# Performance work log

Hardware: AMD Instinct MI355X
Metric: run time of the kernel (lower is better)

## Reference

```python
import jax, jax.numpy as jnp
import numpy as np

B = 512
T = 64
D_MODEL = 1024
N_HEADS = 16
DH = D_MODEL // N_HEADS
GRID_H, GRID_W = 8, 8
DX_MAX, DY_MAX = GRID_W - 1, GRID_H - 1
NUM_REL = (2 * DX_MAX + 1) * (2 * DY_MAX + 1)  # 225


def _build_rel_index():
    # Exactly mirrors RelSelfAttention2DShaw._build_rel_index for an 8x8 board.
    yy, xx = np.meshgrid(np.arange(GRID_H), np.arange(GRID_W), indexing='ij')
    coords = np.stack([xx.reshape(-1), yy.reshape(-1)], axis=-1)  # [T, 2] (x, y)
    disp = coords[None, :, :] - coords[:, None, :]                # [T, T, 2]
    dx = np.clip(disp[..., 0], -DX_MAX, DX_MAX) + DX_MAX
    dy = np.clip(disp[..., 1], -DY_MAX, DY_MAX) + DY_MAX
    return (dx + (2 * DX_MAX + 1) * dy).astype(np.int32)          # [T, T]


def setup_inputs() -> dict:
    key = jax.random.key(0)
    ks = jax.random.split(key, 12)
    w_std = 0.02
    inp = {
        'x':    jax.random.normal(ks[0], (B, T, D_MODEL), dtype=jnp.float32),
        'Wq_w': jax.random.normal(ks[1], (D_MODEL, D_MODEL), dtype=jnp.float32) * w_std,
        'Wq_b': jax.random.normal(ks[2], (D_MODEL,), dtype=jnp.float32) * w_std,
        'Wk_w': jax.random.normal(ks[3], (D_MODEL, D_MODEL), dtype=jnp.float32) * w_std,
        'Wk_b': jax.random.normal(ks[4], (D_MODEL,), dtype=jnp.float32) * w_std,
        'Wv_w': jax.random.normal(ks[5], (D_MODEL, D_MODEL), dtype=jnp.float32) * w_std,
        'Wv_b': jax.random.normal(ks[6], (D_MODEL,), dtype=jnp.float32) * w_std,
        'Wo_w': jax.random.normal(ks[7], (D_MODEL, D_MODEL), dtype=jnp.float32) * w_std,
        'Wo_b': jax.random.normal(ks[8], (D_MODEL,), dtype=jnp.float32) * w_std,
        'rel_q': jax.random.normal(ks[9],  (N_HEADS, NUM_REL, DH), dtype=jnp.float32) * w_std,
        'rel_k': jax.random.normal(ks[10], (N_HEADS, NUM_REL, DH), dtype=jnp.float32) * w_std,
        'rel_v': jax.random.normal(ks[11], (N_HEADS, NUM_REL, DH), dtype=jnp.float32) * w_std,
        'rel_index': jnp.asarray(_build_rel_index()),
    }
    return inp


def reference(x, Wq_w, Wq_b, Wk_w, Wk_b, Wv_w, Wv_b, Wo_w, Wo_b,
              rel_q, rel_k, rel_v, rel_index):
    Bc, Tc, D = x.shape
    H, dh = N_HEADS, DH
    scale = 1.0 / jnp.sqrt(jnp.asarray(dh, dtype=x.dtype))

    # Projections (nn.Linear uses y = x @ W.T + b), split into heads: [B, H, T, dh]
    q = (x @ Wq_w.T + Wq_b).reshape(Bc, Tc, H, dh).transpose(0, 2, 1, 3)
    k = (x @ Wk_w.T + Wk_b).reshape(Bc, Tc, H, dh).transpose(0, 2, 1, 3)
    v = (x @ Wv_w.T + Wv_b).reshape(Bc, Tc, H, dh).transpose(0, 2, 1, 3)

    # Gather per-displacement relative embeddings: [H, T, T, dh]
    rq = rel_q[:, rel_index]
    rk = rel_k[:, rel_index]
    rv = rel_v[:, rel_index]

    # e_ij = (q_i + aQ_ij) . (k_j + aK_ij) / sqrt(dh), expanded into 4 terms
    qk = jnp.einsum('bhtd,bhsd->bhts', q, k)
    q_relk = jnp.einsum('bhtd,htsd->bhts', q, rk)
    relq_k = jnp.einsum('htsd,bhsd->bhts', rq, k)
    relq_relk = jnp.einsum('htsd,htsd->hts', rq, rk)
    logits = (qk + q_relk + relq_k + relq_relk[None]) * scale

    attn = jax.nn.softmax(logits, axis=-1)  # [B, H, T, T]

    # z_i = sum_j attn_ij * (v_j + aV_ij)
    out_v = jnp.einsum('bhts,bhsd->bhtd', attn, v)
    out_relv = jnp.einsum('bhts,htsd->bhtd', attn, rv)
    out = (out_v + out_relv).transpose(0, 2, 1, 3).reshape(Bc, Tc, D)
    return out @ Wo_w.T + Wo_b


if __name__ == '__main__':
    y = reference(**setup_inputs())
    print(y.shape, y.dtype)
```

## Files before the change

kernel.cpp:

```cpp
#include <hip/hip_runtime.h>
#include <cstdint>


typedef unsigned short u16;
typedef unsigned int u32;
typedef __bf16 bf16x8 __attribute__((ext_vector_type(8)));
typedef float f32x4 __attribute__((ext_vector_type(4)));

#define MFMA16(a, b, c) __builtin_amdgcn_mfma_f32_16x16x32_bf16(a, b, c, 0, 0, 0)

__device__ __forceinline__ u16 f2bf(float f) {
  u32 u = __builtin_bit_cast(u32, f);
  u = (u + 0x7FFFu + ((u >> 16) & 1u)) >> 16;
  return (u16)u;
}
__device__ __forceinline__ float bf2f(u16 h) {
  return __builtin_bit_cast(float, ((u32)h) << 16);
}

__device__ __forceinline__ void g2l16(const void* g, void* lds_wave_base) {
#if __has_builtin(__builtin_amdgcn_global_load_lds)
  __builtin_amdgcn_global_load_lds(
      (const __attribute__((address_space(1))) u32*)(uintptr_t)g,
      (__attribute__((address_space(3))) u32*)(uintptr_t)lds_wave_base, 16, 0, 0);
#else
  uint4 v = *(const uint4*)g;
  *(uint4*)((char*)lds_wave_base + (threadIdx.x & 63) * 16) = v;
#endif
}

__global__ __launch_bounds__(256) void k_cvt(const float* __restrict__ src,
                                             u16* __restrict__ dst, int nq) {
  int i = blockIdx.x * 256 + threadIdx.x;
  if (i >= nq) return;
  float4 v = ((const float4*)src)[i];
  ushort4 o;
  o.x = f2bf(v.x); o.y = f2bf(v.y); o.z = f2bf(v.z); o.w = f2bf(v.w);
  ((ushort4*)dst)[i] = o;
}


__device__ __forceinline__ void stageA(const u16* __restrict__ A, int row0,
                                       int kb, char* lds, int buf, int half,
                                       int tid) {
#pragma unroll
  for (int g = 0; g < 2; g++) {
    int ch = g * 512 + tid;
    int sub = ch >> 3, sl = ch & 7;
    int R = (sub & 63) | (half << 6) | ((sub & 64) << 1);
    int kg = sl ^ (sub & 7);
    g2l16(A + (size_t)(row0 + R) * 1024 + kb + kg * 8,
          lds + (buf * 2 + half) * 16384 + g * 8192 + (tid >> 6) * 1024);
  }
}
__device__ __forceinline__ void stageB(const u16* __restrict__ Bm, int col0,
                                       int kb, char* lds, int buf, int half,
                                       int tid) {
#pragma unroll
  for (int g = 0; g < 2; g++) {
    int ch = g * 512 + tid;
    int sub = ch >> 3, sl = ch & 7;
    int C = (sub & 31) | (half << 5) | ((sub & 0x60) << 1);
    int kg = sl ^ (sub & 7);
    g2l16(Bm + (size_t)(col0 + C) * 1024 + kb + kg * 8,
          lds + 65536 + (buf * 2 + half) * 16384 + g * 8192 + (tid >> 6) * 1024);
  }
}

template <int CBUF, int MH, int NH, int RA, int RB, int USEA, int SMAT,
          int SHALF, int SBUF, int KADD, int VMn>
__device__ __forceinline__ void phz(const u16* __restrict__ A,
                                    const u16* __restrict__ Bm, int row0,
                                    int col0, int k0, char* lds,
                                    f32x4 (&acc)[8][4], bf16x8 (&afA)[4][2],
                                    bf16x8 (&afC)[4][2], bf16x8 (&bfB)[2][2],
                                    const int* abase, const int* bbase,
                                    int tid, bool st) {
  if (RA) {
#pragma unroll
    for (int m = 0; m < 4; m++)
#pragma unroll
      for (int kk = 0; kk < 2; kk++) {
        bf16x8 v = *(const bf16x8*)(lds + abase[kk] +
                                    ((CBUF * 2 + MH) * 16384 + m * 2048));
        if (RA == 1) afA[m][kk] = v; else afC[m][kk] = v;
      }
  }
  if (RB) {
#pragma unroll
    for (int n = 0; n < 2; n++)
#pragma unroll
      for (int kk = 0; kk < 2; kk++)
        bfB[n][kk] = *(const bf16x8*)(lds + bbase[kk] +
                                      ((CBUF * 2 + NH) * 16384 + n * 2048));
  }
  if (st) {
    if (SMAT == 0)
      stageA(A, row0, k0 + KADD * 64, lds, SBUF, SHALF, tid);
    else
      stageB(Bm, col0, k0 + KADD * 64, lds, SBUF, SHALF, tid);
  }
  __builtin_amdgcn_s_barrier();
  asm volatile("s_waitcnt lgkmcnt(0)" ::: "memory");
  __builtin_amdgcn_sched_barrier(0);
  __builtin_amdgcn_s_setprio(1);
#pragma unroll
  for (int m = 0; m < 4; m++)
#pragma unroll
    for (int n = 0; n < 2; n++)
#pragma unroll
      for (int kk = 0; kk < 2; kk++)
        acc[MH * 4 + m][NH * 2 + n] = MFMA16(USEA ? afC[m][kk] : afA[m][kk],
                                             bfB[n][kk],
                                             acc[MH * 4 + m][NH * 2 + n]);
  __builtin_amdgcn_s_setprio(0);
  if constexpr (VMn == 8) asm volatile("s_waitcnt vmcnt(8)" ::: "memory");
  else if constexpr (VMn == 6) asm volatile("s_waitcnt vmcnt(6)" ::: "memory");
  else if constexpr (VMn == 4) asm volatile("s_waitcnt vmcnt(4)" ::: "memory");
  else if constexpr (VMn == 2) asm volatile("s_waitcnt vmcnt(2)" ::: "memory");
  else if constexpr (VMn == 0) asm volatile("s_waitcnt vmcnt(0)" ::: "memory");
  __builtin_amdgcn_s_barrier();
}

__device__ __forceinline__ void gemm256_core(const u16* __restrict__ A,
                                             const u16* __restrict__ Bm,
                                             int row0, int col0, char* lds,
                                             f32x4 (&acc)[8][4], int tid) {
  const int lane = tid & 63, w = tid >> 6;
  const int wr = w >> 2, wc = w & 3;
  const int l15 = lane & 15, l4 = lane >> 4;
  const int l7 = l15 & 7;
  int abase[2], bbase[2];
#pragma unroll
  for (int kk = 0; kk < 2; kk++) {
    int swz = ((kk * 4 + l4) ^ l7) << 4;
    abase[kk] = wr * 8192 + l15 * 128 + swz;
    bbase[kk] = 65536 + wc * 4096 + l15 * 128 + swz;
  }
  bf16x8 afA[4][2], afC[4][2], bfB[2][2];
  stageA(A, row0, 0, lds, 0, 0, tid);
  stageB(Bm, col0, 0, lds, 0, 0, tid);
  stageA(A, row0, 0, lds, 0, 1, tid);
  stageB(Bm, col0, 0, lds, 0, 1, tid);
  stageB(Bm, col0, 64, lds, 1, 0, tid);
  stageA(A, row0, 64, lds, 1, 1, tid);
  asm volatile("s_waitcnt vmcnt(4)" ::: "memory");
  __builtin_amdgcn_s_barrier();
  for (int u = 0; u < 7; ++u) {
    int k0 = u * 128;
    phz<0,0,0,1,1,0, 0,0,1,1,-1>(A,Bm,row0,col0,k0,lds,acc,afA,afC,bfB,abase,bbase,tid,true);
    phz<0,1,0,2,0,1, 1,1,1,1, 8>(A,Bm,row0,col0,k0,lds,acc,afA,afC,bfB,abase,bbase,tid,true);
    phz<0,1,1,0,1,1, 1,0,0,2,-1>(A,Bm,row0,col0,k0,lds,acc,afA,afC,bfB,abase,bbase,tid,true);
    phz<0,0,1,0,0,0, 0,1,0,2, 6>(A,Bm,row0,col0,k0,lds,acc,afA,afC,bfB,abase,bbase,tid,true);
    phz<1,0,0,1,1,0, 0,0,0,2,-1>(A,Bm,row0,col0,k0,lds,acc,afA,afC,bfB,abase,bbase,tid,true);
    phz<1,1,0,2,0,1, 1,1,0,2, 8>(A,Bm,row0,col0,k0,lds,acc,afA,afC,bfB,abase,bbase,tid,true);
    phz<1,1,1,0,1,1, 1,0,1,3,-1>(A,Bm,row0,col0,k0,lds,acc,afA,afC,bfB,abase,bbase,tid,true);
    phz<1,0,1,0,0,0, 0,1,1,3, 6>(A,Bm,row0,col0,k0,lds,acc,afA,afC,bfB,abase,bbase,tid,true);
  }
  {
    const int k0 = 896;
    phz<0,0,0,1,1,0, 0,0,1,1,-1>(A,Bm,row0,col0,k0,lds,acc,afA,afC,bfB,abase,bbase,tid,true);
    phz<0,1,0,2,0,1, 1,1,1,1, 8>(A,Bm,row0,col0,k0,lds,acc,afA,afC,bfB,abase,bbase,tid,true);
    phz<0,1,1,0,1,1, 0,0,0,0,-1>(A,Bm,row0,col0,k0,lds,acc,afA,afC,bfB,abase,bbase,tid,false);
    phz<0,0,1,0,0,0, 0,0,0,0, 2>(A,Bm,row0,col0,k0,lds,acc,afA,afC,bfB,abase,bbase,tid,false);
    phz<1,0,0,1,1,0, 0,0,0,0,-1>(A,Bm,row0,col0,k0,lds,acc,afA,afC,bfB,abase,bbase,tid,false);
    phz<1,1,0,2,0,1, 0,0,0,0, 0>(A,Bm,row0,col0,k0,lds,acc,afA,afC,bfB,abase,bbase,tid,false);
    phz<1,1,1,0,1,1, 0,0,0,0,-1>(A,Bm,row0,col0,k0,lds,acc,afA,afC,bfB,abase,bbase,tid,false);
    phz<1,0,1,0,0,0, 0,0,0,0,-1>(A,Bm,row0,col0,k0,lds,acc,afA,afC,bfB,abase,bbase,tid,false);
  }
}

__global__ __launch_bounds__(512, 2) void k_gemm_qkv(
    const u16* __restrict__ A, const u16* __restrict__ Bm,
    const float* __restrict__ bq, const float* __restrict__ bk,
    const float* __restrict__ bv, u16* __restrict__ Qb, u16* __restrict__ Kb,
    u16* __restrict__ Vb) {
  __shared__ char lds[131072];
  const int tid = threadIdx.x;
  const int lane = tid & 63, w = tid >> 6;
  const int wr = w >> 2, wc = w & 3;
  const int l15 = lane & 15, l4 = lane >> 4;
  int f = blockIdx.x;
  int swz = (f & 7) * 192 + (f >> 3);
  int bcol = swz % 12, brow = swz / 12;
  const int row0 = brow * 256, col0 = bcol * 256;
  f32x4 acc[8][4] = {};
  gemm256_core(A, Bm, row0, col0, lds, acc, tid);
  char* eb = lds + w * 16384;
  const int colW = col0 + wc * 64;
  const int sel = colW >> 10, hd = colW & 1023;
  const int h = hd >> 6;
  const float* bp = (sel == 0) ? bq : (sel == 1) ? bk : bv;
  const float* biasW = bp + hd;
  u16* dstW = (sel == 0) ? Qb : (sel == 1) ? Kb : Vb;
#pragma unroll
  for (int r = 0; r < 4; r++) {
#pragma unroll
    for (int mm = 0; mm < 2; mm++) {
      int mf = r * 2 + mm;
#pragma unroll
      for (int nf = 0; nf < 4; nf++)
#pragma unroll
        for (int j = 0; j < 4; j++) {
          int rowl = mm * 16 + l4 * 4 + j;
          *(float*)(eb + rowl * 272 + (nf * 16 + l15) * 4) = acc[mf][nf][j];
        }
    }
    asm volatile("s_waitcnt lgkmcnt(0)" ::: "memory");
    __builtin_amdgcn_sched_barrier(0);
#pragma unroll
    for (int it = 0; it < 4; it++) {
      int u = it * 64 + lane;
      int rowl = u >> 3, ch = u & 7;
      float4 a0 = *(const float4*)(eb + rowl * 272 + ch * 32);
      float4 a1 = *(const float4*)(eb + rowl * 272 + ch * 32 + 16);
      float4 b0 = *(const float4*)(biasW + ch * 8);
      float4 b1 = *(const float4*)(biasW + ch * 8 + 4);
      uint4 pk;
      pk.x = (u32)f2bf(a0.x + b0.x) | ((u32)f2bf(a0.y + b0.y) << 16);
      pk.y = (u32)f2bf(a0.z + b0.z) | ((u32)f2bf(a0.w + b0.w) << 16);
      pk.z = (u32)f2bf(a1.x + b1.x) | ((u32)f2bf(a1.y + b1.y) << 16);
      pk.w = (u32)f2bf(a1.z + b1.z) | ((u32)f2bf(a1.w + b1.w) << 16);
      int row = row0 + wr * 128 + r * 32 + rowl;
      int b = row >> 6, t = row & 63;
      *(uint4*)(dstW + ((size_t)(b * 16 + h)) * 4096 + t * 64 + ch * 8) = pk;
    }
    asm volatile("s_waitcnt lgkmcnt(0)" ::: "memory");
    __builtin_amdgcn_sched_barrier(0);
  }
}

__global__ __launch_bounds__(512, 2) void k_gemm_out(
    const u16* __restrict__ A, const u16* __restrict__ Bm,
    const float* __restrict__ bo, float* __restrict__ out) {
  __shared__ char lds[131072];
  const int tid = threadIdx.x;
  const int lane = tid & 63, w = tid >> 6;
  const int wr = w >> 2, wc = w & 3;
  const int l15 = lane & 15, l4 = lane >> 4;
  int f = blockIdx.x;
  int swz = (f & 7) * 64 + (f >> 3);
  int bcol = swz & 3, brow = swz >> 2;
  const int row0 = brow * 256, col0 = bcol * 256;
  f32x4 acc[8][4] = {};
  gemm256_core(A, Bm, row0, col0, lds, acc, tid);
  char* eb = lds + w * 16384;
  const int colW = col0 + wc * 64;
  const float* biasW = bo + colW;
#pragma unroll
  for (int r = 0; r < 4; r++) {
#pragma unroll
    for (int mm = 0; mm < 2; mm++) {
      int mf = r * 2 + mm;
#pragma unroll
      for (int nf = 0; nf < 4; nf++)
#pragma unroll
        for (int j = 0; j < 4; j++) {
          int rowl = mm * 16 + l4 * 4 + j;
          *(float*)(eb + rowl * 272 + (nf * 16 + l15) * 4) = acc[mf][nf][j];
        }
    }
    asm volatile("s_waitcnt lgkmcnt(0)" ::: "memory");
    __builtin_amdgcn_sched_barrier(0);
#pragma unroll
    for (int it = 0; it < 8; it++) {
      int u = it * 64 + lane;
      int rowl = u >> 4, ch = u & 15;
      float4 a0 = *(const float4*)(eb + rowl * 272 + ch * 16);
      float4 b0 = *(const float4*)(biasW + ch * 4);
      a0.x += b0.x; a0.y += b0.y; a0.z += b0.z; a0.w += b0.w;
      int row = row0 + wr * 128 + r * 32 + rowl;
      *(float4*)(out + (size_t)row * 1024 + colW + ch * 4) = a0;
    }
    asm volatile("s_waitcnt lgkmcnt(0)" ::: "memory");
    __builtin_amdgcn_sched_barrier(0);
  }
}

__global__ __launch_bounds__(256) void k_bias1(
    const u16* __restrict__ Qb, const u16* __restrict__ relq,
    const u16* __restrict__ relk, const int* __restrict__ relidx,
    u16* __restrict__ bias1) {
  const int tid = threadIdx.x, lane = tid & 63, w = tid >> 6;
  const int l15 = lane & 15, l4 = lane >> 4;
  const int t = blockIdx.x, h = blockIdx.y, bc = blockIdx.z;
  __shared__ char lds[16640];
  char* RK = lds;
  char* RQ = lds + 8192;
  float* T3 = (float*)(lds + 16384);
#pragma unroll
  for (int c = 0; c < 2; c++) {
    int ch = c * 256 + tid;
    int sr = ch >> 3, sl = (ch & 7) ^ (sr & 7);
    int ri = relidx[t * 64 + sr];
    size_t so = ((size_t)h * 225 + ri) * 64 + sl * 8;
    g2l16(relk + so, RK + c * 4096 + w * 1024);
    g2l16(relq + so, RQ + c * 4096 + w * 1024);
  }
  __syncthreads();
  if (tid < 64) {
    int sr = tid;
    float sum = 0.f;
#pragma unroll
    for (int sl = 0; sl < 8; sl++) {
      int o = sr * 128 + ((sl ^ (sr & 7)) << 4);
      bf16x8 aq = *(const bf16x8*)(RQ + o);
      bf16x8 ak = *(const bf16x8*)(RK + o);
#pragma unroll
      for (int j = 0; j < 8; j++) sum += (float)aq[j] * (float)ak[j];
    }
    T3[sr] = sum;
  }
  bf16x8 bfr[4][2];
#pragma unroll
  for (int n = 0; n < 4; n++)
#pragma unroll
    for (int kh = 0; kh < 2; kh++) {
      int r = n * 16 + l15;
      int sl = ((kh << 2) + l4) ^ (r & 7);
      bfr[n][kh] = *(const bf16x8*)(RK + r * 128 + sl * 16);
    }
  __syncthreads();
  f32x4 acc[4][4] = {};
#pragma unroll
  for (int m = 0; m < 4; m++) {
    int bb = bc * 256 + w * 64 + m * 16 + l15;
    const u16* ap = Qb + ((size_t)(bb * 16 + h)) * 4096 + t * 64 + l4 * 8;
    bf16x8 a0 = *(const bf16x8*)ap;
    bf16x8 a1 = *(const bf16x8*)(ap + 32);
#pragma unroll
    for (int n = 0; n < 4; n++) {
      acc[m][n] = MFMA16(a0, bfr[n][0], acc[m][n]);
      acc[m][n] = MFMA16(a1, bfr[n][1], acc[m][n]);
    }
  }
#pragma unroll
  for (int m = 0; m < 4; m++)
#pragma unroll
    for (int n = 0; n < 4; n++)
#pragma unroll
      for (int j = 0; j < 4; j++) {
        int bb = bc * 256 + w * 64 + m * 16 + l4 * 4 + j;
        int s_ = n * 16 + l15;
        bias1[((size_t)(bb * 16 + h)) * 4096 + t * 64 + s_] =
            f2bf(acc[m][n][j] + T3[s_]);
      }
}

__global__ __launch_bounds__(256) void k_bias2(
    const u16* __restrict__ Kb, const u16* __restrict__ relq,
    const int* __restrict__ relidx, u16* __restrict__ bias2) {
  const int tid = threadIdx.x, lane = tid & 63, w = tid >> 6;
  const int l15 = lane & 15, l4 = lane >> 4;
  const int s = blockIdx.x, h = blockIdx.y, bc = blockIdx.z;
  __shared__ char lds[8192];
#pragma unroll
  for (int c = 0; c < 2; c++) {
    int ch = c * 256 + tid;
    int tq = ch >> 3, sl = (ch & 7) ^ (tq & 7);
    int ri = relidx[tq * 64 + s];
    g2l16(relq + ((size_t)h * 225 + ri) * 64 + sl * 8,
          lds + c * 4096 + w * 1024);
  }
  __syncthreads();
  bf16x8 bfr[4][2];
#pragma unroll
  for (int n = 0; n < 4; n++)
#pragma unroll
    for (int kh = 0; kh < 2; kh++) {
      int r = n * 16 + l15;
      int sl = ((kh << 2) + l4) ^ (r & 7);
      bfr[n][kh] = *(const bf16x8*)(lds + r * 128 + sl * 16);
    }
  f32x4 acc[4][4] = {};
#pragma unroll
  for (int m = 0; m < 4; m++) {
    int bb = bc * 256 + w * 64 + m * 16 + l15;
    const u16* ap = Kb + ((size_t)(bb * 16 + h)) * 4096 + s * 64 + l4 * 8;
    bf16x8 a0 = *(const bf16x8*)ap;
    bf16x8 a1 = *(const bf16x8*)(ap + 32);
#pragma unroll
    for (int n = 0; n < 4; n++) {
      acc[m][n] = MFMA16(a0, bfr[n][0], acc[m][n]);
      acc[m][n] = MFMA16(a1, bfr[n][1], acc[m][n]);
    }
  }
#pragma unroll
  for (int m = 0; m < 4; m++)
#pragma unroll
    for (int n = 0; n < 4; n++)
#pragma unroll
      for (int j = 0; j < 4; j++) {
        int bb = bc * 256 + w * 64 + m * 16 + l4 * 4 + j;
        int tcol = n * 16 + l15;
        bias2[((size_t)(bb * 16 + h)) * 4096 + s * 64 + tcol] =
            f2bf(acc[m][n][j]);
      }
}

__global__ __launch_bounds__(256) void k_attn(
    const u16* __restrict__ Qb, const u16* __restrict__ Kb,
    const u16* __restrict__ Vb, const u16* __restrict__ b1g,
    const u16* __restrict__ b2g, u16* __restrict__ Pg,
    u16* __restrict__ aout) {
  const int tid = threadIdx.x, lane = tid & 63, w = tid >> 6;
  const int l15 = lane & 15, l4 = lane >> 4;
  const int b = blockIdx.x, h = blockIdx.y;
  __shared__ char lds[49152];
  char* Qt = lds;
  char* Kt = lds + 8192;
  char* Vt = lds + 16384;
  char* B1 = lds + 24576;
  char* B2 = lds + 32768;
  char* Pt = lds + 40960;
  const size_t base = ((size_t)(b * 16 + h)) * 4096;
#pragma unroll
  for (int c = 0; c < 2; c++) {
    int ch = c * 256 + tid;
    int r = ch >> 3, sl = (ch & 7) ^ (r & 7);
    size_t so = base + r * 64 + sl * 8;
    int dst = c * 4096 + w * 1024;
    g2l16(Qb + so, Qt + dst);
    g2l16(Kb + so, Kt + dst);
    g2l16(Vb + so, Vt + dst);
    g2l16(b1g + so, B1 + dst);
    g2l16(b2g + so, B2 + dst);
  }
  __syncthreads();
  f32x4 acc[4] = {};
  bf16x8 qf[2];
  {
    int r = w * 16 + l15;
#pragma unroll
    for (int kh = 0; kh < 2; kh++) {
      int sl = ((kh << 2) + l4) ^ (r & 7);
      qf[kh] = *(const bf16x8*)(Qt + r * 128 + sl * 16);
    }
  }
#pragma unroll
  for (int n = 0; n < 4; n++) {
    int r = n * 16 + l15;
#pragma unroll
    for (int kh = 0; kh < 2; kh++) {
      int sl = ((kh << 2) + l4) ^ (r & 7);
      bf16x8 kf = *(const bf16x8*)(Kt + r * 128 + sl * 16);
      acc[n] = MFMA16(qf[kh], kf, acc[n]);
    }
  }
  const int t0 = w * 16 + l4 * 4;
#pragma unroll
  for (int j = 0; j < 4; j++) {
    int t_ = t0 + j;
    float lv[4];
#pragma unroll
    for (int n = 0; n < 4; n++) {
      int s_ = n * 16 + l15;
      float x = acc[n][j];
      x += bf2f(*(const u16*)(B1 + t_ * 128 + ((s_ * 2) ^ ((t_ & 7) << 4))));
      x += bf2f(*(const u16*)(B2 + s_ * 128 + ((t_ * 2) ^ ((s_ & 7) << 4))));
      lv[n] = x * 0.125f;
    }
    float mx = fmaxf(fmaxf(lv[0], lv[1]), fmaxf(lv[2], lv[3]));
#pragma unroll
    for (int d = 1; d < 16; d <<= 1) mx = fmaxf(mx, __shfl_xor(mx, d, 64));
    float e0 = __expf(lv[0] - mx), e1 = __expf(lv[1] - mx);
    float e2 = __expf(lv[2] - mx), e3 = __expf(lv[3] - mx);
    float sum = e0 + e1 + e2 + e3;
#pragma unroll
    for (int d = 1; d < 16; d <<= 1) sum += __shfl_xor(sum, d, 64);
    float inv = 1.0f / sum;
    float pe[4] = {e0 * inv, e1 * inv, e2 * inv, e3 * inv};
#pragma unroll
    for (int n = 0; n < 4; n++) {
      int s_ = n * 16 + l15;
      *(u16*)(Pt + t_ * 128 + ((s_ * 2) ^ ((t_ & 7) << 4))) = f2bf(pe[n]);
    }
  }
  __syncthreads();
#pragma unroll
  for (int c = 0; c < 2; c++) {
    int ch = c * 256 + tid;
    int r = ch >> 3, sl = ch & 7;
    uint4 v = *(const uint4*)(Pt + r * 128 + ((sl ^ (r & 7)) << 4));
    *((uint4*)(Pg + base) + ch) = v;
  }
  f32x4 acc2[4] = {};
  bf16x8 pf[2];
  {
    int r = w * 16 + l15;
#pragma unroll
    for (int kh = 0; kh < 2; kh++) {
      int sl = ((kh << 2) + l4) ^ (r & 7);
      pf[kh] = *(const bf16x8*)(Pt + r * 128 + sl * 16);
    }
  }
#pragma unroll
  for (int n = 0; n < 4; n++) {
#pragma unroll
    for (int kh = 0; kh < 2; kh++) {
      bf16x8 tmp;
#pragma unroll
      for (int j = 0; j < 8; j++) {
        int s_ = (kh << 5) + (l4 << 3) + j;
        int d_ = n * 16 + l15;
        u16 uu = *(const u16*)(Vt + s_ * 128 + ((d_ * 2) ^ ((s_ & 7) << 4)));
        tmp[j] = __builtin_bit_cast(__bf16, uu);
      }
      acc2[n] = MFMA16(pf[kh], tmp, acc2[n]);
    }
  }
#pragma unroll
  for (int n = 0; n < 4; n++)
#pragma unroll
    for (int j = 0; j < 4; j++) {
      int t_ = t0 + j, d_ = n * 16 + l15;
      aout[((size_t)(b * 64 + t_)) * 1024 + h * 64 + d_] = f2bf(acc2[n][j]);
    }
}

__global__ __launch_bounds__(256) void k_relv(
    const u16* __restrict__ Pg, const u16* __restrict__ relv,
    const int* __restrict__ relidx, u16* __restrict__ aout) {
  const int tid = threadIdx.x, lane = tid & 63, w = tid >> 6;
  const int l15 = lane & 15, l4 = lane >> 4;
  const int t = blockIdx.x, h = blockIdx.y, bc = blockIdx.z;
  __shared__ char lds[8192];
#pragma unroll
  for (int c = 0; c < 2; c++) {
    int ch = c * 256 + tid;
    int sr = ch >> 3, sl = (ch & 7) ^ (sr & 7);
    int ri = relidx[t * 64 + sr];
    g2l16(relv + ((size_t)h * 225 + ri) * 64 + sl * 8,
          lds + c * 4096 + w * 1024);
  }
  __syncthreads();
  bf16x8 bfr[4][2];
#pragma unroll
  for (int n = 0; n < 4; n++)
#pragma unroll
    for (int kh = 0; kh < 2; kh++) {
      bf16x8 tmp;
#pragma unroll
      for (int j = 0; j < 8; j++) {
        int s_ = (kh << 5) + (l4 << 3) + j;
        int d_ = n * 16 + l15;
        u16 u = *(const u16*)(lds + s_ * 128 + ((d_ * 2) ^ ((s_ & 7) << 4)));
        tmp[j] = __builtin_bit_cast(__bf16, u);
      }
      bfr[n][kh] = tmp;
    }
  f32x4 acc[4][4] = {};
#pragma unroll
  for (int m = 0; m < 4; m++) {
    int bb = bc * 256 + w * 64 + m * 16 + l15;
    const u16* ap = Pg + ((size_t)(bb * 16 + h)) * 4096 + t * 64 + l4 * 8;
    bf16x8 a0 = *(const bf16x8*)ap;
    bf16x8 a1 = *(const bf16x8*)(ap + 32);
#pragma unroll
    for (int n = 0; n < 4; n++) {
      acc[m][n] = MFMA16(a0, bfr[n][0], acc[m][n]);
      acc[m][n] = MFMA16(a1, bfr[n][1], acc[m][n]);
    }
  }
#pragma unroll
  for (int m = 0; m < 4; m++)
#pragma unroll
    for (int n = 0; n < 4; n++)
#pragma unroll
      for (int j = 0; j < 4; j++) {
        int bb = bc * 256 + w * 64 + m * 16 + l4 * 4 + j;
        int d_ = n * 16 + l15;
        size_t o = ((size_t)(bb * 64 + t)) * 1024 + h * 64 + d_;
        aout[o] = f2bf(bf2f(aout[o]) + acc[m][n][j]);
      }
}

extern "C" void kernel_launch(void* const* d_in, const int* in_sizes, int n_in,
                              void* d_out, int out_size, void* d_ws,
                              size_t ws_size, hipStream_t stream) {
  const float* x = (const float*)d_in[0];
  const float* Wq = (const float*)d_in[1];
  const float* bq = (const float*)d_in[2];
  const float* Wk = (const float*)d_in[3];
  const float* bk = (const float*)d_in[4];
  const float* Wv = (const float*)d_in[5];
  const float* bv = (const float*)d_in[6];
  const float* Wo = (const float*)d_in[7];
  const float* bo = (const float*)d_in[8];
  const float* rq = (const float*)d_in[9];
  const float* rk = (const float*)d_in[10];
  const float* rv = (const float*)d_in[11];
  const int* ridx = (const int*)d_in[12];
  float* out = (float*)d_out;

  char* ws = (char*)d_ws;
  const size_t MB = 1ull << 20;
  u16* xb = (u16*)(ws + 0);
  u16* Qb = (u16*)(ws + 64 * MB);
  u16* Kb = (u16*)(ws + 128 * MB);
  u16* Vb = (u16*)(ws + 192 * MB);
  u16* b1 = (u16*)(ws + 256 * MB);
  u16* b2 = (u16*)(ws + 320 * MB);
  u16* aout = (u16*)(ws + 384 * MB);
  u16* wqkv = (u16*)(ws + 448 * MB);
  u16* wo = (u16*)(ws + 454 * MB);
  u16* relq = (u16*)(ws + 456 * MB);
  u16* relk = (u16*)(ws + 457 * MB);
  u16* relv = (u16*)(ws + 458 * MB);
  u16* Pg = xb;

  k_cvt<<<32768, 256, 0, stream>>>(x, xb, 8388608);
  k_cvt<<<1024, 256, 0, stream>>>(Wq, wqkv, 262144);
  k_cvt<<<1024, 256, 0, stream>>>(Wk, wqkv + 1048576, 262144);
  k_cvt<<<1024, 256, 0, stream>>>(Wv, wqkv + 2097152, 262144);
  k_cvt<<<1024, 256, 0, stream>>>(Wo, wo, 262144);
  k_cvt<<<225, 256, 0, stream>>>(rq, relq, 57600);
  k_cvt<<<225, 256, 0, stream>>>(rk, relk, 57600);
  k_cvt<<<225, 256, 0, stream>>>(rv, relv, 57600);

  k_gemm_qkv<<<1536, 512, 0, stream>>>(xb, wqkv, bq, bk, bv, Qb, Kb, Vb);
  k_bias1<<<dim3(64, 16, 2), 256, 0, stream>>>(Qb, relq, relk, ridx, b1);
  k_bias2<<<dim3(64, 16, 2), 256, 0, stream>>>(Kb, relq, ridx, b2);
  k_attn<<<dim3(512, 16), 256, 0, stream>>>(Qb, Kb, Vb, b1, b2, Pg, aout);
  k_relv<<<dim3(64, 16, 2), 256, 0, stream>>>(Pg, relv, ridx, aout);
  k_gemm_out<<<512, 512, 0, stream>>>(aout, wo, bo, out);
}
```

Measured before the change: 548.3 us.

## Restructure GEMM main loop into six phases with precomputed staging pointers

Replaces the eight-phase templated pipeline with six phases per 128-wide K step. Two of the phases now issue both MFMA quadrants back to back, reusing the loaded A fragments and cutting barriers per iteration. Global-to-LDS staging addresses are precomputed once as per-thread byte pointers, so index arithmetic in the loop reduces to adding an offset. The prologue now waits for all loads (vmcnt 0), and the vmcnt wait counts are retuned, which risks exposing more load latency or ordering hazards.

```diff
diff --git a/kernel.cpp b/kernel.cpp
--- a/kernel.cpp
+++ b/kernel.cpp
@@ -40,79 +40,42 @@
 }
 
 
-__device__ __forceinline__ void stageA(const u16* __restrict__ A, int row0,
-                                       int kb, char* lds, int buf, int half,
-                                       int tid) {
-#pragma unroll
-  for (int g = 0; g < 2; g++) {
-    int ch = g * 512 + tid;
-    int sub = ch >> 3, sl = ch & 7;
-    int R = (sub & 63) | (half << 6) | ((sub & 64) << 1);
-    int kg = sl ^ (sub & 7);
-    g2l16(A + (size_t)(row0 + R) * 1024 + kb + kg * 8,
-          lds + (buf * 2 + half) * 16384 + g * 8192 + (tid >> 6) * 1024);
-  }
-}
-__device__ __forceinline__ void stageB(const u16* __restrict__ Bm, int col0,
-                                       int kb, char* lds, int buf, int half,
-                                       int tid) {
-#pragma unroll
-  for (int g = 0; g < 2; g++) {
-    int ch = g * 512 + tid;
-    int sub = ch >> 3, sl = ch & 7;
-    int C = (sub & 31) | (half << 5) | ((sub & 0x60) << 1);
-    int kg = sl ^ (sub & 7);
-    g2l16(Bm + (size_t)(col0 + C) * 1024 + kb + kg * 8,
-          lds + 65536 + (buf * 2 + half) * 16384 + g * 8192 + (tid >> 6) * 1024);
-  }
-}
-
-template <int CBUF, int MH, int NH, int RA, int RB, int USEA, int SMAT,
-          int SHALF, int SBUF, int KADD, int VMn>
-__device__ __forceinline__ void phz(const u16* __restrict__ A,
-                                    const u16* __restrict__ Bm, int row0,
-                                    int col0, int k0, char* lds,
-                                    f32x4 (&acc)[8][4], bf16x8 (&afA)[4][2],
-                                    bf16x8 (&afC)[4][2], bf16x8 (&bfB)[2][2],
-                                    const int* abase, const int* bbase,
-                                    int tid, bool st) {
-  if (RA) {
-#pragma unroll
-    for (int m = 0; m < 4; m++)
-#pragma unroll
-      for (int kk = 0; kk < 2; kk++) {
-        bf16x8 v = *(const bf16x8*)(lds + abase[kk] +
-                                    ((CBUF * 2 + MH) * 16384 + m * 2048));
-        if (RA == 1) afA[m][kk] = v; else afC[m][kk] = v;
-      }
-  }
-  if (RB) {
+template <int OFF>
+__device__ __forceinline__ void rdAf(const char* lds, const int* abase,
+                                     bf16x8 (&f)[4][2]) {
+#pragma unroll
+  for (int m = 0; m < 4; m++)
+#pragma unroll
+    for (int kk = 0; kk < 2; kk++)
+      f[m][kk] = *(const bf16x8*)(lds + abase[kk] + OFF + m * 2048);
+}
+template <int OFF>
+__device__ __forceinline__ void rdBf(const char* lds, const int* bbase,
+                                     bf16x8 (&f)[2][2]) {
+#pragma unroll
+  for (int n = 0; n < 2; n++)
+#pragma unroll
+    for (int kk = 0; kk < 2; kk++)
+      f[n][kk] = *(const bf16x8*)(lds + bbase[kk] + OFF + n * 2048);
+}
+__device__ __forceinline__ void mq(f32x4 (&acc)[8][4], const bf16x8 (&af)[4][2],
+                                   const bf16x8 (&bf)[2][2], int MR, int NC) {
+#pragma unroll
+  for (int m = 0; m < 4; m++)
 #pragma unroll
     for (int n = 0; n < 2; n++)
 #pragma unroll
       for (int kk = 0; kk < 2; kk++)
-        bfB[n][kk] = *(const bf16x8*)(lds + bbase[kk] +
-                                      ((CBUF * 2 + NH) * 16384 + n * 2048));
-  }
-  if (st) {
-    if (SMAT == 0)
-      stageA(A, row0, k0 + KADD * 64, lds, SBUF, SHALF, tid);
-    else
-      stageB(Bm, col0, k0 + KADD * 64, lds, SBUF, SHALF, tid);
-  }
+        acc[MR + m][NC + n] = MFMA16(af[m][kk], bf[n][kk], acc[MR + m][NC + n]);
+}
+__device__ __forceinline__ void ph_begin() {
   __builtin_amdgcn_s_barrier();
   asm volatile("s_waitcnt lgkmcnt(0)" ::: "memory");
   __builtin_amdgcn_sched_barrier(0);
   __builtin_amdgcn_s_setprio(1);
-#pragma unroll
-  for (int m = 0; m < 4; m++)
-#pragma unroll
-    for (int n = 0; n < 2; n++)
-#pragma unroll
-      for (int kk = 0; kk < 2; kk++)
-        acc[MH * 4 + m][NH * 2 + n] = MFMA16(USEA ? afC[m][kk] : afA[m][kk],
-                                             bfB[n][kk],
-                                             acc[MH * 4 + m][NH * 2 + n]);
+}
+template <int VMn>
+__device__ __forceinline__ void ph_end() {
   __builtin_amdgcn_s_setprio(0);
   if constexpr (VMn == 8) asm volatile("s_waitcnt vmcnt(8)" ::: "memory");
   else if constexpr (VMn == 6) asm volatile("s_waitcnt vmcnt(6)" ::: "memory");
@@ -120,6 +83,11 @@
   else if constexpr (VMn == 2) asm volatile("s_waitcnt vmcnt(2)" ::: "memory");
   else if constexpr (VMn == 0) asm volatile("s_waitcnt vmcnt(0)" ::: "memory");
   __builtin_amdgcn_s_barrier();
+}
+__device__ __forceinline__ void st2(const char* p0, const char* p1, int off,
+                                    char* lds, int dst, int woff) {
+  g2l16(p0 + off, lds + dst + woff);
+  g2l16(p1 + off, lds + dst + 8192 + woff);
 }
 
 __device__ __forceinline__ void gemm256_core(const u16* __restrict__ A,
@@ -137,36 +105,71 @@
     abase[kk] = wr * 8192 + l15 * 128 + swz;
     bbase[kk] = 65536 + wc * 4096 + l15 * 128 + swz;
   }
+  const int sub0 = tid >> 3, sl0 = tid & 7;
+  const int sub1 = (512 + tid) >> 3, sl1 = tid & 7;
+  const int woff = w * 1024;
+  const char* pa0 = (const char*)A + (size_t)row0 * 2048 +
+      (size_t)((sub0 & 63) | ((sub0 & 64) << 1)) * 2048 + (sl0 ^ (sub0 & 7)) * 16;
+  const char* pa1 = (const char*)A + (size_t)row0 * 2048 +
+      (size_t)((sub1 & 63) | ((sub1 & 64) << 1)) * 2048 + (sl1 ^ (sub1 & 7)) * 16;
+  const char* pb0 = (const char*)Bm + (size_t)col0 * 2048 +
+      (size_t)((sub0 & 31) | ((sub0 & 0x60) << 1)) * 2048 + (sl0 ^ (sub0 & 7)) * 16;
+  const char* pb1 = (const char*)Bm + (size_t)col0 * 2048 +
+      (size_t)((sub1 & 31) | ((sub1 & 0x60) << 1)) * 2048 + (sl1 ^ (sub1 & 7)) * 16;
+
   bf16x8 afA[4][2], afC[4][2], bfB[2][2];
-  stageA(A, row0, 0, lds, 0, 0, tid);
-  stageB(Bm, col0, 0, lds, 0, 0, tid);
-  stageA(A, row0, 0, lds, 0, 1, tid);
-  stageB(Bm, col0, 0, lds, 0, 1, tid);
-  stageB(Bm, col0, 64, lds, 1, 0, tid);
-  stageA(A, row0, 64, lds, 1, 1, tid);
-  asm volatile("s_waitcnt vmcnt(4)" ::: "memory");
+
+  st2(pa0, pa1, 0, lds, 0, woff);
+  st2(pb0, pb1, 0, lds, 65536, woff);
+  st2(pa0, pa1, 131072, lds, 16384, woff);
+  st2(pb0, pb1, 65536, lds, 65536 + 16384, woff);
+  st2(pb0, pb1, 128, lds, 65536 + 32768, woff);
+  st2(pa0, pa1, 131072 + 128, lds, 49152, woff);
+  asm volatile("s_waitcnt vmcnt(0)" ::: "memory");
   __builtin_amdgcn_s_barrier();
+
   for (int u = 0; u < 7; ++u) {
-    int k0 = u * 128;
-    phz<0,0,0,1,1,0, 0,0,1,1,-1>(A,Bm,row0,col0,k0,lds,acc,afA,afC,bfB,abase,bbase,tid,true);
-    phz<0,1,0,2,0,1, 1,1,1,1, 8>(A,Bm,row0,col0,k0,lds,acc,afA,afC,bfB,abase,bbase,tid,true);
-    phz<0,1,1,0,1,1, 1,0,0,2,-1>(A,Bm,row0,col0,k0,lds,acc,afA,afC,bfB,abase,bbase,tid,true);
-    phz<0,0,1,0,0,0, 0,1,0,2, 6>(A,Bm,row0,col0,k0,lds,acc,afA,afC,bfB,abase,bbase,tid,true);
-    phz<1,0,0,1,1,0, 0,0,0,2,-1>(A,Bm,row0,col0,k0,lds,acc,afA,afC,bfB,abase,bbase,tid,true);
-    phz<1,1,0,2,0,1, 1,1,0,2, 8>(A,Bm,row0,col0,k0,lds,acc,afA,afC,bfB,abase,bbase,tid,true);
-    phz<1,1,1,0,1,1, 1,0,1,3,-1>(A,Bm,row0,col0,k0,lds,acc,afA,afC,bfB,abase,bbase,tid,true);
-    phz<1,0,1,0,0,0, 0,1,1,3, 6>(A,Bm,row0,col0,k0,lds,acc,afA,afC,bfB,abase,bbase,tid,true);
+    const int kB = u * 256;
+    rdAf<0>(lds, abase, afA);
+    rdBf<0>(lds, bbase, bfB);
+    st2(pa0, pa1, kB + 128, lds, 32768, woff);
+    ph_begin(); mq(acc, afA, bfB, 0, 0); ph_end<-1>();
+    rdAf<16384>(lds, abase, afC);
+    st2(pb0, pb1, 65536 + kB + 128, lds, 65536 + 49152, woff);
+    ph_begin(); mq(acc, afC, bfB, 4, 0); ph_end<-1>();
+    rdBf<16384>(lds, bbase, bfB);
+    st2(pb0, pb1, kB + 256, lds, 65536, woff);
+    st2(pa0, pa1, 131072 + kB + 256, lds, 16384, woff);
+    ph_begin(); mq(acc, afC, bfB, 4, 2); mq(acc, afA, bfB, 0, 2); ph_end<6>();
+    rdAf<32768>(lds, abase, afA);
+    rdBf<32768>(lds, bbase, bfB);
+    st2(pa0, pa1, kB + 256, lds, 0, woff);
+    ph_begin(); mq(acc, afA, bfB, 0, 0); ph_end<-1>();
+    rdAf<49152>(lds, abase, afC);
+    st2(pb0, pb1, 65536 + kB + 256, lds, 65536 + 16384, woff);
+    ph_begin(); mq(acc, afC, bfB, 4, 0); ph_end<8>();
+    rdBf<49152>(lds, bbase, bfB);
+    st2(pb0, pb1, kB + 384, lds, 65536 + 32768, woff);
+    st2(pa0, pa1, 131072 + kB + 384, lds, 49152, woff);
+    ph_begin(); mq(acc, afC, bfB, 4, 2); mq(acc, afA, bfB, 0, 2); ph_end<4>();
   }
   {
-    const int k0 = 896;
-    phz<0,0,0,1,1,0, 0,0,1,1,-1>(A,Bm,row0,col0,k0,lds,acc,afA,afC,bfB,abase,bbase,tid,true);
-    phz<0,1,0,2,0,1, 1,1,1,1, 8>(A,Bm,row0,col0,k0,lds,acc,afA,afC,bfB,abase,bbase,tid,true);
-    phz<0,1,1,0,1,1, 0,0,0,0,-1>(A,Bm,row0,col0,k0,lds,acc,afA,afC,bfB,abase,bbase,tid,false);
-    phz<0,0,1,0,0,0, 0,0,0,0, 2>(A,Bm,row0,col0,k0,lds,acc,afA,afC,bfB,abase,bbase,tid,false);
-    phz<1,0,0,1,1,0, 0,0,0,0,-1>(A,Bm,row0,col0,k0,lds,acc,afA,afC,bfB,abase,bbase,tid,false);
-    phz<1,1,0,2,0,1, 0,0,0,0, 0>(A,Bm,row0,col0,k0,lds,acc,afA,afC,bfB,abase,bbase,tid,false);
-    phz<1,1,1,0,1,1, 0,0,0,0,-1>(A,Bm,row0,col0,k0,lds,acc,afA,afC,bfB,abase,bbase,tid,false);
-    phz<1,0,1,0,0,0, 0,0,0,0,-1>(A,Bm,row0,col0,k0,lds,acc,afA,afC,bfB,abase,bbase,tid,false);
+    rdAf<0>(lds, abase, afA);
+    rdBf<0>(lds, bbase, bfB);
+    st2(pa0, pa1, 1792 + 128, lds, 32768, woff);
+    ph_begin(); mq(acc, afA, bfB, 0, 0); ph_end<-1>();
+    rdAf<16384>(lds, abase, afC);
+    st2(pb0, pb1, 65536 + 1792 + 128, lds, 65536 + 49152, woff);
+    ph_begin(); mq(acc, afC, bfB, 4, 0); ph_end<-1>();
+    rdBf<16384>(lds, bbase, bfB);
+    ph_begin(); mq(acc, afC, bfB, 4, 2); mq(acc, afA, bfB, 0, 2); ph_end<2>();
+    rdAf<32768>(lds, abase, afA);
+    rdBf<32768>(lds, bbase, bfB);
+    ph_begin(); mq(acc, afA, bfB, 0, 0); ph_end<-1>();
+    rdAf<49152>(lds, abase, afC);
+    ph_begin(); mq(acc, afC, bfB, 4, 0); ph_end<0>();
+    rdBf<49152>(lds, bbase, bfB);
+    ph_begin(); mq(acc, afC, bfB, 4, 2); mq(acc, afA, bfB, 0, 2); ph_end<-1>();
   }
 }
 
```

Result: faster. 534.9 us (-2.4%).
